# Kernel tuning notes

Measured on AMD Instinct MI355X. Metric: run time of the kernel, lower is better.

Reference implementation:

```python
import jax, jax.numpy as jnp
import numpy as np

N, E, D, H = 20000, 320000, 128, 256
NUM_FINE = 2


def _mlp(x, W1, b1, W2, b2):
    # Linear -> relu -> Linear -> relu (dropout rate 0.0 is identity)
    h = jax.nn.relu(x @ W1 + b1)
    return jax.nn.relu(h @ W2 + b2)


def setup_inputs() -> dict:
    key = jax.random.key(0)
    ks = jax.random.split(key, 12)

    def p(k, shape):
        fan_in = shape[0]
        return jax.random.normal(k, shape, jnp.float32) * (1.0 / fan_in) ** 0.5

    return {
        "nodes": jax.random.normal(ks[0], (N, D), jnp.float32),
        "edges": jax.random.normal(ks[1], (E, D), jnp.float32),
        "senders": jax.random.randint(ks[2], (E,), 0, N, jnp.int32),
        "receivers": jax.random.randint(ks[3], (E,), 0, N, jnp.int32),
        # embed node MLP: D -> H -> D
        "Wn1": p(ks[4], (D, H)), "bn1": jnp.zeros((H,), jnp.float32),
        "Wn2": p(ks[5], (H, D)), "bn2": jnp.zeros((D,), jnp.float32),
        # embed edge MLP: D -> H -> D
        "We1": p(ks[6], (D, H)), "be1": jnp.zeros((H,), jnp.float32),
        "We2": p(ks[7], (H, D)), "be2": jnp.zeros((D,), jnp.float32),
        # edge model MLP: 3D -> H -> D  (concat[src, dest, edge_attr])
        "Wed1": p(ks[8], (3 * D, H)), "bed1": jnp.zeros((H,), jnp.float32),
        "Wed2": p(ks[9], (H, D)), "bed2": jnp.zeros((D,), jnp.float32),
        # node model MLP: 2D -> H -> D  (concat[x, segment_sum(edge_attr)])
        "Wnd1": p(ks[10], (2 * D, H)), "bnd1": jnp.zeros((H,), jnp.float32),
        "Wnd2": p(ks[11], (H, D)), "bnd2": jnp.zeros((D,), jnp.float32),
    }


def reference(nodes, edges, senders, receivers,
              Wn1, bn1, Wn2, bn2, We1, be1, We2, be2,
              Wed1, bed1, Wed2, bed2, Wnd1, bnd1, Wnd2, bnd2):
    # Embed stage (EmbedMetaLayer)
    x = _mlp(nodes, Wn1, bn1, Wn2, bn2)   # (N, D)
    e = _mlp(edges, We1, be1, We2, be2)   # (E, D)

    pooled = []
    for _ in range(NUM_FINE):
        # EdgeModel: gather src/dest node feats, concat with edge feats, MLP
        edge_in = jnp.concatenate([x[senders], x[receivers], e], axis=-1)  # (E, 3D)
        e = _mlp(edge_in, Wed1, bed1, Wed2, bed2)                           # (E, D)
        # NodeModel: scatter-add edge feats to receiver nodes, concat, MLP
        agg = jax.ops.segment_sum(e, receivers, num_segments=N)            # (N, D)
        x = _mlp(jnp.concatenate([x, agg], axis=-1), Wnd1, bnd1, Wnd2, bnd2)  # (N, D)
        # global_add_pooling: vmap(jnp.sum) over nodes -> per-node feature sum (N,)
        pooled.append(jnp.sum(x, axis=-1))
    # concatenate along last axis of the 1-D pooled vectors -> (NUM_FINE * N,)
    return jnp.concatenate(pooled, axis=-1)
```

## Files before the change

kernel.cpp:

```cpp
#include <hip/hip_runtime.h>
#include <stdint.h>

#define N_NODES 20000
#define N_EDGES 320000

typedef __attribute__((ext_vector_type(8)))  __bf16        bf16x8;
typedef __attribute__((ext_vector_type(16))) float         f32x16;
typedef __attribute__((ext_vector_type(4)))  float         f32x4v;
typedef __attribute__((ext_vector_type(4)))  uint32_t      u32x4;
typedef __attribute__((ext_vector_type(8)))  unsigned short us8;
typedef __attribute__((ext_vector_type(2)))  unsigned short us2;

static __device__ __forceinline__ unsigned short cvt_bf16(float f) {
  uint32_t u = __builtin_bit_cast(uint32_t, f);
  u = (u + 0x7fffu + ((u >> 16) & 1u)) >> 16;
  return (unsigned short)u;
}
static __device__ __forceinline__ float cvt_f32(unsigned short h) {
  uint32_t u = ((uint32_t)h) << 16;
  return __builtin_bit_cast(float, u);
}

static __device__ __forceinline__ void gll16(const void* g, void* l) {
  __builtin_amdgcn_global_load_lds(
      (const __attribute__((address_space(1))) unsigned int*)g,
      (__attribute__((address_space(3))) unsigned int*)l, 16, 0, 0);
}

__global__ void pack_w(const float* __restrict__ W, unsigned short* __restrict__ out,
                       int K, int Ncols) {
  int idx = blockIdx.x * 256 + threadIdx.x;
  int total = K * Ncols;
  if (idx >= total) return;
  int e    = idx & 7;
  int lane = (idx >> 3) & 63;
  int t    = idx >> 9;
  int ntiles = Ncols >> 5;
  int nt = t % ntiles;
  int ks = t / ntiles;
  int k = ks * 16 + (lane >> 5) * 8 + e;
  int c = nt * 32 + (lane & 31);
  out[idx] = cvt_bf16(W[(size_t)k * Ncols + c]);
}

__global__ void pack_w2(const float* __restrict__ W, unsigned short* __restrict__ out) {
  int idx = blockIdx.x * 256 + threadIdx.x;
  if (idx >= 32768) return;
  int e    = idx & 7;
  int lane = (idx >> 3) & 63;
  int t    = idx >> 9;
  int nt = t & 3, ks = t >> 2;
  int k = ks * 16 + ((lane >> 5) << 2) + (e & 3) + ((e >> 2) << 3);
  int c = nt * 32 + (lane & 31);
  out[idx] = cvt_bf16(W[(size_t)k * 128 + c]);
}

__global__ void hist_k(const int* __restrict__ recv, int* __restrict__ cnt, int n) {
  int i = blockIdx.x * 256 + threadIdx.x;
  if (i < n) atomicAdd(&cnt[recv[i]], 1);
}

__global__ void scan_k(const int* __restrict__ cnt, int* __restrict__ off,
                       int* __restrict__ cursor, int n) {
  __shared__ int part[1024];
  int t = threadIdx.x;
  int chunk = (n + 1023) / 1024;
  int base = t * chunk;
  int s = 0;
  for (int i = 0; i < chunk; ++i) { int idx = base + i; if (idx < n) s += cnt[idx]; }
  part[t] = s;
  __syncthreads();
  for (int d = 1; d < 1024; d <<= 1) {
    int v = (t >= d) ? part[t - d] : 0;
    __syncthreads();
    part[t] += v;
    __syncthreads();
  }
  int prefix = (t > 0) ? part[t - 1] : 0;
  for (int i = 0; i < chunk; ++i) {
    int idx = base + i;
    if (idx < n) { off[idx] = prefix; cursor[idx] = prefix; prefix += cnt[idx]; }
  }
  if (t == 1023) off[n] = part[1023];
}

__global__ void fill_k(const int* __restrict__ recv, int* __restrict__ cursor,
                       int* __restrict__ eid, int n) {
  int i = blockIdx.x * 256 + threadIdx.x;
  if (i < n) {
    int p = atomicAdd(&cursor[recv[i]], 1);
    eid[p] = i;
  }
}

__global__ void agg_k(const unsigned short* __restrict__ eb, const int* __restrict__ off,
                      const int* __restrict__ eid, unsigned short* __restrict__ aggb, int n) {
  int node = blockIdx.x * 4 + (threadIdx.x >> 6);
  if (node >= n) return;
  int lane = threadIdx.x & 63;
  float a0 = 0.f, a1 = 0.f;
  int s = off[node], t = off[node + 1];
  for (int q = s; q < t; ++q) {
    int ei = eid[q];
    us2 v = *(const us2*)(eb + (size_t)ei * 128 + lane * 2);
    a0 += cvt_f32(v[0]);
    a1 += cvt_f32(v[1]);
  }
  us2 r; r[0] = cvt_bf16(a0); r[1] = cvt_bf16(a1);
  *(us2*)(aggb + (size_t)node * 128 + lane * 2) = r;
}

template <int KIN, int MODE, int POOL>
__global__ __launch_bounds__(256, 2)
void mlp_kernel(const float* __restrict__ srcf,
                const unsigned short* __restrict__ xb,
                const unsigned short* __restrict__ ebuf,
                const unsigned short* __restrict__ aggb,
                const int* __restrict__ senders,
                const int* __restrict__ receivers,
                const unsigned short* __restrict__ P1,
                const float* __restrict__ b1,
                const unsigned short* __restrict__ P2,
                const float* __restrict__ b2,
                unsigned short* __restrict__ dst,
                float* __restrict__ pool_out,
                int nrows) {
  constexpr int NS1 = KIN / 32;
  __shared__ __align__(16) unsigned char lds[32768];

  const int tid  = threadIdx.x;
  const int lane = tid & 63;
  const int wid  = tid >> 6;
  const int g    = lane >> 5;
  const int l31  = lane & 31;
  const int rowBlock = blockIdx.x << 7;

  const unsigned char* P1b = (const unsigned char*)P1;

  int grow = rowBlock + wid * 32 + l31;
  if (grow >= nrows) grow = nrows - 1;

  const unsigned short *pS = nullptr, *pR = nullptr, *pE = nullptr;
  const unsigned short *pX = nullptr, *pAg = nullptr;
  const float* fb = nullptr;
  if constexpr (MODE == 0) {
    fb = srcf + (size_t)grow * KIN;
  } else if constexpr (MODE == 1) {
    pS = xb + (size_t)senders[grow] * 128;
    pR = xb + (size_t)receivers[grow] * 128;
    pE = ebuf + (size_t)grow * 128;
  } else {
    pX  = xb + (size_t)grow * 128;
    pAg = aggb + (size_t)grow * 128;
  }

  auto STG1 = [&](int s) {
    unsigned char* bW = lds + (s & 1) * 16384;
#pragma unroll
    for (int c = 0; c < 4; ++c)
      gll16(P1b + (size_t)s * 16384 + c * 4096 + tid * 16,
            bW + c * 4096 + wid * 1024);
  };

  auto LROW = [&](int s, us8& o0, us8& o1) {
    const int k0s = s * 32;
    const unsigned short* p;
    if constexpr (MODE == 1) {
      const int seg = k0s >> 7;
      p = (seg == 0) ? pS : (seg == 1) ? pR : pE;
    } else {
      p = (k0s >> 7) ? pAg : pX;
    }
    const int ko = k0s & 127;
    o0 = *(const us8*)(p + ko + g * 8);
    o1 = *(const us8*)(p + ko + 16 + g * 8);
  };
  auto LROWF = [&](int s, f32x4v* rf) {
    const float* p = fb + s * 32 + g * 8;
    rf[0] = *(const f32x4v*)(p);
    rf[1] = *(const f32x4v*)(p + 4);
    rf[2] = *(const f32x4v*)(p + 16);
    rf[3] = *(const f32x4v*)(p + 20);
  };
  auto MKBR = [&](const f32x4v* rf, bf16x8& b0v, bf16x8& b1v) {
    us8 h0, h1;
#pragma unroll
    for (int e = 0; e < 4; ++e) {
      h0[e] = cvt_bf16(rf[0][e]); h0[4 + e] = cvt_bf16(rf[1][e]);
      h1[e] = cvt_bf16(rf[2][e]); h1[4 + e] = cvt_bf16(rf[3][e]);
    }
    b0v = __builtin_bit_cast(bf16x8, h0);
    b1v = __builtin_bit_cast(bf16x8, h1);
  };

  f32x16 acc1[8];
#pragma unroll
  for (int t = 0; t < 8; ++t)
#pragma unroll
    for (int k = 0; k < 16; ++k) acc1[t][k] = 0.0f;

  auto COMPUTE = [&](const unsigned char* bW, bf16x8 b0v, bf16x8 b1v) {
#pragma unroll
    for (int kc = 0; kc < 2; ++kc) {
      const bf16x8 bv = kc ? b1v : b0v;
#pragma unroll
      for (int nt = 0; nt < 8; ++nt) {
        bf16x8 av = __builtin_bit_cast(bf16x8,
            *(const us8*)(bW + (kc * 8 + nt) * 1024 + lane * 16));
        acc1[nt] = __builtin_amdgcn_mfma_f32_32x32x16_bf16(av, bv, acc1[nt], 0, 0, 0);
      }
    }
  };

  constexpr int CNT = (MODE == 0) ? 8 : 6;

  us8 rA0, rA1, rB0, rB1;
  f32x4v rfA[4], rfB[4];

  STG1(0);
  if constexpr (MODE == 0) LROWF(0, rfA); else LROW(0, rA0, rA1);

#pragma unroll 1
  for (int s = 0; s < NS1; s += 2) {
    STG1(s + 1);
    if constexpr (MODE == 0) LROWF(s + 1, rfB); else LROW(s + 1, rB0, rB1);
    asm volatile("s_waitcnt vmcnt(%0)" :: "i"(CNT) : "memory");
    asm volatile("s_barrier" ::: "memory");
    {
      bf16x8 b0v, b1v;
      if constexpr (MODE == 0) MKBR(rfA, b0v, b1v);
      else { b0v = __builtin_bit_cast(bf16x8, rA0); b1v = __builtin_bit_cast(bf16x8, rA1); }
      COMPUTE(lds, b0v, b1v);
    }
    asm volatile("s_waitcnt lgkmcnt(0)" ::: "memory");
    asm volatile("s_barrier" ::: "memory");

    const bool more = (s + 2 < NS1);
    if (more) {
      STG1(s + 2);
      if constexpr (MODE == 0) LROWF(s + 2, rfA); else LROW(s + 2, rA0, rA1);
      asm volatile("s_waitcnt vmcnt(%0)" :: "i"(CNT) : "memory");
    } else {
      asm volatile("s_waitcnt vmcnt(0)" ::: "memory");
    }
    asm volatile("s_barrier" ::: "memory");
    {
      bf16x8 b0v, b1v;
      if constexpr (MODE == 0) MKBR(rfB, b0v, b1v);
      else { b0v = __builtin_bit_cast(bf16x8, rB0); b1v = __builtin_bit_cast(bf16x8, rB1); }
      COMPUTE(lds + 16384, b0v, b1v);
    }
    if (more) {
      asm volatile("s_waitcnt lgkmcnt(0)" ::: "memory");
      asm volatile("s_barrier" ::: "memory");
    }
  }

  u32x4 pa4[16];
#pragma unroll
  for (int t = 0; t < 8; ++t) {
#pragma unroll
    for (int q4 = 0; q4 < 4; ++q4) {
      const f32x4v bb = *(const f32x4v*)(b1 + t * 32 + q4 * 8 + g * 4);
      float v0 = fmaxf(acc1[t][q4 * 4 + 0] + bb[0], 0.0f);
      float v1 = fmaxf(acc1[t][q4 * 4 + 1] + bb[1], 0.0f);
      float v2 = fmaxf(acc1[t][q4 * 4 + 2] + bb[2], 0.0f);
      float v3 = fmaxf(acc1[t][q4 * 4 + 3] + bb[3], 0.0f);
      uint32_t lo, hi;
      asm("v_cvt_pk_bf16_f32 %0, %1, %2" : "=v"(lo) : "v"(v0), "v"(v1));
      asm("v_cvt_pk_bf16_f32 %0, %1, %2" : "=v"(hi) : "v"(v2), "v"(v3));
      pa4[t * 2 + (q4 >> 1)][(q4 & 1) * 2 + 0] = lo;
      pa4[t * 2 + (q4 >> 1)][(q4 & 1) * 2 + 1] = hi;
    }
  }

  f32x16 acc2[4];
#pragma unroll
  for (int nt = 0; nt < 4; ++nt)
#pragma unroll
    for (int k = 0; k < 16; ++k) acc2[nt][k] = 0.0f;

#pragma unroll
  for (int ks = 0; ks < 16; ++ks) {
    const bf16x8 a2 = __builtin_bit_cast(bf16x8, pa4[ks]);
#pragma unroll
    for (int nt = 0; nt < 4; ++nt) {
      const bf16x8 bw = __builtin_bit_cast(bf16x8,
          *(const us8*)(P2 + (size_t)((ks * 4 + nt) * 64 + lane) * 8));
      acc2[nt] = __builtin_amdgcn_mfma_f32_32x32x16_bf16(a2, bw, acc2[nt], 0, 0, 0);
    }
  }

  float bias2[4];
#pragma unroll
  for (int nt = 0; nt < 4; ++nt) bias2[nt] = b2[nt * 32 + l31];

#pragma unroll
  for (int reg = 0; reg < 16; ++reg) {
    const int rowpat = (reg & 3) + ((reg >> 2) << 3) + g * 4;
    const int row = rowBlock + wid * 32 + rowpat;
    float vs = 0.0f;
#pragma unroll
    for (int nt = 0; nt < 4; ++nt) {
      float v = fmaxf(acc2[nt][reg] + bias2[nt], 0.0f);
      vs += v;
      if (row < nrows) dst[(size_t)row * 128 + nt * 32 + l31] = cvt_bf16(v);
    }
    if constexpr (POOL) {
#pragma unroll
      for (int m = 1; m <= 16; m <<= 1) vs += __shfl_xor(vs, m, 64);
      if (l31 == 0 && row < nrows) pool_out[row] = vs;
    }
  }
}

static constexpr size_t OFF_X    = 0;
static constexpr size_t OFF_E    = 5120000;
static constexpr size_t OFF_AGG  = 87040000;
static constexpr size_t OFF_PN1  = 92160000;
static constexpr size_t OFF_PN2  = OFF_PN1 + 65536;
static constexpr size_t OFF_PE1  = OFF_PN2 + 65536;
static constexpr size_t OFF_PE2  = OFF_PE1 + 65536;
static constexpr size_t OFF_PD1  = OFF_PE2 + 65536;
static constexpr size_t OFF_PD2  = OFF_PD1 + 196608;
static constexpr size_t OFF_PM1  = OFF_PD2 + 65536;
static constexpr size_t OFF_PM2  = OFF_PM1 + 131072;
static constexpr size_t OFF_CNT  = OFF_PM2 + 65536;
static constexpr size_t OFF_OFFS = OFF_CNT + 80000;
static constexpr size_t OFF_CUR  = OFF_OFFS + 80004;
static constexpr size_t OFF_EID  = OFF_CUR + 80000;

extern "C" void kernel_launch(void* const* d_in, const int* in_sizes, int n_in,
                              void* d_out, int out_size, void* d_ws, size_t ws_size,
                              hipStream_t stream) {
  const float* nodes = (const float*)d_in[0];
  const float* edges = (const float*)d_in[1];
  const int* senders = (const int*)d_in[2];
  const int* receivers = (const int*)d_in[3];
  const float* Wn1 = (const float*)d_in[4];  const float* bn1 = (const float*)d_in[5];
  const float* Wn2 = (const float*)d_in[6];  const float* bn2 = (const float*)d_in[7];
  const float* We1 = (const float*)d_in[8];  const float* be1 = (const float*)d_in[9];
  const float* We2 = (const float*)d_in[10]; const float* be2 = (const float*)d_in[11];
  const float* Wed1 = (const float*)d_in[12]; const float* bed1 = (const float*)d_in[13];
  const float* Wed2 = (const float*)d_in[14]; const float* bed2 = (const float*)d_in[15];
  const float* Wnd1 = (const float*)d_in[16]; const float* bnd1 = (const float*)d_in[17];
  const float* Wnd2 = (const float*)d_in[18]; const float* bnd2 = (const float*)d_in[19];

  char* ws = (char*)d_ws;
  unsigned short* xb   = (unsigned short*)(ws + OFF_X);
  unsigned short* eb   = (unsigned short*)(ws + OFF_E);
  unsigned short* aggb = (unsigned short*)(ws + OFF_AGG);
  unsigned short* Pn1  = (unsigned short*)(ws + OFF_PN1);
  unsigned short* Pn2  = (unsigned short*)(ws + OFF_PN2);
  unsigned short* Pe1  = (unsigned short*)(ws + OFF_PE1);
  unsigned short* Pe2  = (unsigned short*)(ws + OFF_PE2);
  unsigned short* Pd1  = (unsigned short*)(ws + OFF_PD1);
  unsigned short* Pd2  = (unsigned short*)(ws + OFF_PD2);
  unsigned short* Pm1  = (unsigned short*)(ws + OFF_PM1);
  unsigned short* Pm2  = (unsigned short*)(ws + OFF_PM2);
  int* cnt    = (int*)(ws + OFF_CNT);
  int* offs   = (int*)(ws + OFF_OFFS);
  int* cursor = (int*)(ws + OFF_CUR);
  int* eid    = (int*)(ws + OFF_EID);
  float* outp = (float*)d_out;

  pack_w<<<128, 256, 0, stream>>>(Wn1, Pn1, 128, 256);
  pack_w2<<<128, 256, 0, stream>>>(Wn2, Pn2);
  pack_w<<<128, 256, 0, stream>>>(We1, Pe1, 128, 256);
  pack_w2<<<128, 256, 0, stream>>>(We2, Pe2);
  pack_w<<<384, 256, 0, stream>>>(Wed1, Pd1, 384, 256);
  pack_w2<<<128, 256, 0, stream>>>(Wed2, Pd2);
  pack_w<<<256, 256, 0, stream>>>(Wnd1, Pm1, 256, 256);
  pack_w2<<<128, 256, 0, stream>>>(Wnd2, Pm2);

  hipMemsetAsync(cnt, 0, (size_t)N_NODES * 4, stream);
  hist_k<<<1250, 256, 0, stream>>>(receivers, cnt, N_EDGES);
  scan_k<<<1, 1024, 0, stream>>>(cnt, offs, cursor, N_NODES);
  fill_k<<<1250, 256, 0, stream>>>(receivers, cursor, eid, N_EDGES);

  const int nodeBlocks = (N_NODES + 127) / 128;
  const int edgeBlocks = N_EDGES / 128;

  mlp_kernel<128, 0, 0><<<nodeBlocks, 256, 0, stream>>>(
      nodes, nullptr, nullptr, nullptr, nullptr, nullptr,
      Pn1, bn1, Pn2, bn2, xb, nullptr, N_NODES);
  mlp_kernel<128, 0, 0><<<edgeBlocks, 256, 0, stream>>>(
      edges, nullptr, nullptr, nullptr, nullptr, nullptr,
      Pe1, be1, Pe2, be2, eb, nullptr, N_EDGES);

  for (int it = 0; it < 2; ++it) {
    mlp_kernel<384, 1, 0><<<edgeBlocks, 256, 0, stream>>>(
        nullptr, xb, eb, nullptr, senders, receivers,
        Pd1, bed1, Pd2, bed2, eb, nullptr, N_EDGES);
    agg_k<<<(N_NODES + 3) / 4, 256, 0, stream>>>(eb, offs, eid, aggb, N_NODES);
    mlp_kernel<256, 2, 1><<<nodeBlocks, 256, 0, stream>>>(
        nullptr, xb, nullptr, aggb, nullptr, nullptr,
        Pm1, bnd1, Pm2, bnd2, xb, outp + (size_t)it * N_NODES, N_NODES);
  }
}
```

Before: 526.5 us.

## Stage second-layer MLP weights through LDS with double-buffered async loads

The second GEMM used to read W2 fragments straight from global memory inside its MFMA loop. It now streams W2 in four 16KB chunks into the two LDS buffers with global_load_lds, double-buffered, and each chunk load overlaps the MFMAs on the previous chunk. s_setprio is also raised around the MFMA blocks to favour the compute waves. In exchange there are extra barriers, and an unused bias preload array (bb) adds register pressure.

```diff
diff --git a/kernel.cpp b/kernel.cpp
--- a/kernel.cpp
+++ b/kernel.cpp
@@ -136,6 +136,7 @@
   const int rowBlock = blockIdx.x << 7;
 
   const unsigned char* P1b = (const unsigned char*)P1;
+  const unsigned char* P2b = (const unsigned char*)P2;
 
   int grow = rowBlock + wid * 32 + l31;
   if (grow >= nrows) grow = nrows - 1;
@@ -161,6 +162,13 @@
       gll16(P1b + (size_t)s * 16384 + c * 4096 + tid * 16,
             bW + c * 4096 + wid * 1024);
   };
+  auto STG2 = [&](int c) {
+    unsigned char* bW = lds + (c & 1) * 16384;
+#pragma unroll
+    for (int q = 0; q < 4; ++q)
+      gll16(P2b + (size_t)c * 16384 + q * 4096 + tid * 16,
+            bW + q * 4096 + wid * 1024);
+  };
 
   auto LROW = [&](int s, us8& o0, us8& o1) {
     const int k0s = s * 32;
@@ -200,6 +208,7 @@
     for (int k = 0; k < 16; ++k) acc1[t][k] = 0.0f;
 
   auto COMPUTE = [&](const unsigned char* bW, bf16x8 b0v, bf16x8 b1v) {
+    __builtin_amdgcn_s_setprio(1);
 #pragma unroll
     for (int kc = 0; kc < 2; ++kc) {
       const bf16x8 bv = kc ? b1v : b0v;
@@ -210,6 +219,7 @@
         acc1[nt] = __builtin_amdgcn_mfma_f32_32x32x16_bf16(av, bv, acc1[nt], 0, 0, 0);
       }
     }
+    __builtin_amdgcn_s_setprio(0);
   };
 
   constexpr int CNT = (MODE == 0) ? 8 : 6;
@@ -256,16 +266,26 @@
     }
   }
 
+  f32x4v bb[8];
+#pragma unroll
+  for (int t = 0; t < 8; ++t)
+    bb[t] = *(const f32x4v*)(b1 + t * 32 + (lane & 7) * 4);
+
+  STG2(0);
+  asm volatile("s_waitcnt lgkmcnt(0)" ::: "memory");
+  asm volatile("s_barrier" ::: "memory");
+  STG2(1);
+
   u32x4 pa4[16];
 #pragma unroll
   for (int t = 0; t < 8; ++t) {
 #pragma unroll
     for (int q4 = 0; q4 < 4; ++q4) {
-      const f32x4v bb = *(const f32x4v*)(b1 + t * 32 + q4 * 8 + g * 4);
-      float v0 = fmaxf(acc1[t][q4 * 4 + 0] + bb[0], 0.0f);
-      float v1 = fmaxf(acc1[t][q4 * 4 + 1] + bb[1], 0.0f);
-      float v2 = fmaxf(acc1[t][q4 * 4 + 2] + bb[2], 0.0f);
-      float v3 = fmaxf(acc1[t][q4 * 4 + 3] + bb[3], 0.0f);
+      const f32x4v bv4 = *(const f32x4v*)(b1 + t * 32 + q4 * 8 + g * 4);
+      float v0 = fmaxf(acc1[t][q4 * 4 + 0] + bv4[0], 0.0f);
+      float v1 = fmaxf(acc1[t][q4 * 4 + 1] + bv4[1], 0.0f);
+      float v2 = fmaxf(acc1[t][q4 * 4 + 2] + bv4[2], 0.0f);
+      float v3 = fmaxf(acc1[t][q4 * 4 + 3] + bv4[3], 0.0f);
       uint32_t lo, hi;
       asm("v_cvt_pk_bf16_f32 %0, %1, %2" : "=v"(lo) : "v"(v0), "v"(v1));
       asm("v_cvt_pk_bf16_f32 %0, %1, %2" : "=v"(hi) : "v"(v2), "v"(v3));
@@ -281,14 +301,26 @@
     for (int k = 0; k < 16; ++k) acc2[nt][k] = 0.0f;
 
 #pragma unroll
-  for (int ks = 0; ks < 16; ++ks) {
-    const bf16x8 a2 = __builtin_bit_cast(bf16x8, pa4[ks]);
-#pragma unroll
-    for (int nt = 0; nt < 4; ++nt) {
-      const bf16x8 bw = __builtin_bit_cast(bf16x8,
-          *(const us8*)(P2 + (size_t)((ks * 4 + nt) * 64 + lane) * 8));
-      acc2[nt] = __builtin_amdgcn_mfma_f32_32x32x16_bf16(a2, bw, acc2[nt], 0, 0, 0);
-    }
+  for (int c = 0; c < 4; ++c) {
+    if (c < 3) asm volatile("s_waitcnt vmcnt(4)" ::: "memory");
+    else       asm volatile("s_waitcnt vmcnt(0)" ::: "memory");
+    asm volatile("s_barrier" ::: "memory");
+    const unsigned char* bW = lds + (c & 1) * 16384;
+    __builtin_amdgcn_s_setprio(1);
+#pragma unroll
+    for (int kk = 0; kk < 4; ++kk) {
+      const bf16x8 a2 = __builtin_bit_cast(bf16x8, pa4[c * 4 + kk]);
+#pragma unroll
+      for (int nt = 0; nt < 4; ++nt) {
+        const bf16x8 bw = __builtin_bit_cast(bf16x8,
+            *(const us8*)(bW + (kk * 4 + nt) * 1024 + lane * 16));
+        acc2[nt] = __builtin_amdgcn_mfma_f32_32x32x16_bf16(a2, bw, acc2[nt], 0, 0, 0);
+      }
+    }
+    __builtin_amdgcn_s_setprio(0);
+    asm volatile("s_waitcnt lgkmcnt(0)" ::: "memory");
+    asm volatile("s_barrier" ::: "memory");
+    if (c + 2 < 4) STG2(c + 2);
   }
 
   float bias2[4];
```

Measured after the change: 515.5 us. -2.1%, faster.
